# Performance work log

Hardware: AMD Instinct MI355X
Metric: run time of the kernel (lower is better)

The kernel has to match this reference:

```python
import jax, jax.numpy as jnp
import numpy as np

D_MODEL = 1024
N_HEADS = 16
D_K = 64
B = 2
S = 2048


def setup_inputs() -> dict:
    key = jax.random.key(0)
    ks = jax.random.split(key, 6)
    scale = 1.0 / np.sqrt(D_MODEL)
    x = jax.random.normal(ks[0], (B, S, D_MODEL), dtype=jnp.float32)
    Wq = jax.random.normal(ks[1], (D_MODEL, D_MODEL), dtype=jnp.float32) * scale
    Wk = jax.random.normal(ks[2], (D_MODEL, D_MODEL), dtype=jnp.float32) * scale
    Wv = jax.random.normal(ks[3], (D_MODEL, D_MODEL), dtype=jnp.float32) * scale
    Wo = jax.random.normal(ks[4], (D_MODEL, D_MODEL), dtype=jnp.float32) * scale
    bq = jnp.zeros((D_MODEL,), jnp.float32)
    bk = jnp.zeros((D_MODEL,), jnp.float32)
    bv = jnp.zeros((D_MODEL,), jnp.float32)
    bo = jnp.zeros((D_MODEL,), jnp.float32)
    # causal mask, broadcast over batch and heads: [1, 1, S, S]
    mask = jnp.tril(jnp.ones((S, S), jnp.int32))[None, None, :, :]
    return {"x": x, "mask": mask, "Wq": Wq, "bq": bq, "Wk": Wk, "bk": bk,
            "Wv": Wv, "bv": bv, "Wo": Wo, "bo": bo}


def reference(x, mask, Wq, bq, Wk, bk, Wv, bv, Wo, bo):
    b, s, _ = x.shape
    # projections (torch Linear: y = x @ W^T + b); split heads -> [b, h, s, d_k]
    def split_heads(y):
        return y.reshape(b, s, N_HEADS, D_K).transpose(0, 2, 1, 3)
    Q = split_heads(x @ Wq.T + bq)
    K = split_heads(x @ Wk.T + bk)
    V = split_heads(x @ Wv.T + bv)
    scores = jnp.einsum('bhqd,bhkd->bhqk', Q, K) / jnp.sqrt(jnp.float32(D_K))
    scores = jnp.where(mask == 0, -jnp.inf, scores)
    attn = jax.nn.softmax(scores, axis=-1)  # dropout p=0 -> identity
    out = jnp.einsum('bhqk,bhkd->bhqd', attn, V)
    out = out.transpose(0, 2, 1, 3).reshape(b, s, D_MODEL)
    return out @ Wo.T + bo
```

## Files before the change

kernel.cpp:

```cpp
#include <hip/hip_runtime.h>
#include <math.h>
#include <type_traits>

#define D_MODEL 1024
#define N_HEADS 16
#define D_KK    64
#define B_SZ    2
#define SEQ     2048
#define M_TOTAL (B_SZ * SEQ)

#define QSCALE 0.18033688011112042f

typedef __attribute__((ext_vector_type(8))) short short8;
typedef __attribute__((ext_vector_type(4))) float f32x4;

static __device__ __forceinline__ ushort f2bf(float f) {
    union { float f; unsigned u; } c; c.f = f;
    unsigned u = c.u;
    unsigned r = (u + 0x7fffu + ((u >> 16) & 1u)) >> 16;
    return (ushort)r;
}

static __device__ __forceinline__ unsigned packbf(float a, float b) {
    unsigned ua = __float_as_uint(a) + 0x8000u;
    unsigned ub = __float_as_uint(b) + 0x8000u;
    return __builtin_amdgcn_perm(ub, ua, 0x07060302u);
}

static __device__ __forceinline__ void gload16(const void* g, void* l) {
    __builtin_amdgcn_global_load_lds(
        (const __attribute__((address_space(1))) void*)g,
        (__attribute__((address_space(3))) void*)l, 16, 0, 0);
}

__global__ __launch_bounds__(256)
void cvt_kernel(const float* __restrict__ x,  const float* __restrict__ wq,
                const float* __restrict__ wk, const float* __restrict__ wv,
                const float* __restrict__ wo,
                ushort* __restrict__ xb,  ushort* __restrict__ wqb,
                ushort* __restrict__ wkb, ushort* __restrict__ wvb,
                ushort* __restrict__ wob)
{
    const float* s; ushort* d; int n4;
    switch (blockIdx.y) {
        case 0:  s = x;  d = xb;  n4 = M_TOTAL * D_MODEL / 4; break;
        case 1:  s = wq; d = wqb; n4 = D_MODEL * D_MODEL / 4; break;
        case 2:  s = wk; d = wkb; n4 = D_MODEL * D_MODEL / 4; break;
        case 3:  s = wv; d = wvb; n4 = D_MODEL * D_MODEL / 4; break;
        default: s = wo; d = wob; n4 = D_MODEL * D_MODEL / 4; break;
    }
    const int stride = gridDim.x * blockDim.x;
    for (int i = blockIdx.x * blockDim.x + threadIdx.x; i < n4; i += stride) {
        float4 v = reinterpret_cast<const float4*>(s)[i];
        ushort4 u;
        u.x = f2bf(v.x); u.y = f2bf(v.y); u.z = f2bf(v.z); u.w = f2bf(v.w);
        reinterpret_cast<ushort4*>(d)[i] = u;
    }
}

template<int EPI>
__global__ __launch_bounds__(256)
void gemm_mfma(const ushort* __restrict__ A,
               const ushort* __restrict__ W0, const float* __restrict__ b0, void* __restrict__ C0,
               const ushort* __restrict__ W1, const float* __restrict__ b1, void* __restrict__ C1,
               const ushort* __restrict__ W2, const float* __restrict__ b2, void* __restrict__ C2)
{
    constexpr int K = D_MODEL;

    const ushort* W    = W0;
    const float*  bias = b0;
    void*         C    = C0;
    if (blockIdx.z == 1) { W = W1; bias = b1; C = C1; }
    else if (blockIdx.z == 2) { W = W2; bias = b2; C = C2; }

    __shared__ ushort As[128 * 32];
    __shared__ ushort Bs[128 * 32];

    const int tid  = threadIdx.x;
    const int w    = tid >> 6;
    const int lane = tid & 63;
    const int lr   = lane & 15;
    const int lc   = lane >> 4;
    const int wr   = w >> 1;
    const int wc   = w & 1;
    const int m0   = blockIdx.x * 128;
    const int n0   = blockIdx.y * 128;

    const int srow = lane >> 2;
    const int scol = (lane & 3) * 8;
    const int g0   = w * 2;

    const ushort* gA = A + (size_t)(m0 + g0 * 16 + srow) * K + scol;
    const ushort* gB = W + (size_t)(n0 + g0 * 16 + srow) * K + scol;
    ushort* lA = &As[g0 * 512];
    ushort* lB = &Bs[g0 * 512];

    f32x4 acc[4][4];
#pragma unroll
    for (int m = 0; m < 4; ++m)
#pragma unroll
        for (int n = 0; n < 4; ++n) acc[m][n] = (f32x4)0.0f;

    for (int k0 = 0; k0 < K; k0 += 32) {
        gload16(gA + k0,          lA);
        gload16(gA + k0 + 16 * K, lA + 512);
        gload16(gB + k0,          lB);
        gload16(gB + k0 + 16 * K, lB + 512);
        __syncthreads();

        short8 af[4], bfr[4];
#pragma unroll
        for (int m = 0; m < 4; ++m)
            af[m] = *reinterpret_cast<const short8*>(
                &As[(wr * 64 + m * 16 + lr) * 32 + lc * 8]);
#pragma unroll
        for (int n = 0; n < 4; ++n)
            bfr[n] = *reinterpret_cast<const short8*>(
                &Bs[(wc * 64 + n * 16 + lr) * 32 + lc * 8]);
#pragma unroll
        for (int m = 0; m < 4; ++m)
#pragma unroll
            for (int n = 0; n < 4; ++n)
                acc[m][n] = __builtin_amdgcn_mfma_f32_16x16x32_bf16(
                    af[m], bfr[n], acc[m][n], 0, 0, 0);
        __syncthreads();
    }

    float bv[4];
#pragma unroll
    for (int n = 0; n < 4; ++n) bv[n] = bias[n0 + wc * 64 + n * 16 + lr];
    const int row_base = m0 + wr * 64;

    if (EPI == 0) {
        float* Cf = (float*)C;
#pragma unroll
        for (int m = 0; m < 4; ++m)
#pragma unroll
        for (int r = 0; r < 4; ++r) {
            const int row = row_base + m * 16 + lc * 4 + r;
#pragma unroll
            for (int n = 0; n < 4; ++n)
                Cf[(size_t)row * D_MODEL + n0 + wc * 64 + n * 16 + lr] =
                    acc[m][n][r] + bv[n];
        }
    } else {
        ushort* Cu = (ushort*)C;
        const bool vt  = (blockIdx.z == 2);
        const float osc = (blockIdx.z == 0) ? QSCALE : 1.0f;
#pragma unroll
        for (int m = 0; m < 4; ++m) {
            const int row4 = row_base + m * 16 + lc * 4;
            const int bb = row4 >> 11;
            const int ss = row4 & 2047;
            const size_t bhbase = (size_t)bb * N_HEADS;
#pragma unroll
            for (int n = 0; n < 4; ++n) {
                const int col = n0 + wc * 64 + n * 16 + lr;
                const int h = col >> 6, d = col & 63;
                if (vt) {
                    ushort4 u;
                    u.x = f2bf(acc[m][n][0] + bv[n]);
                    u.y = f2bf(acc[m][n][1] + bv[n]);
                    u.z = f2bf(acc[m][n][2] + bv[n]);
                    u.w = f2bf(acc[m][n][3] + bv[n]);
                    *reinterpret_cast<ushort4*>(
                        &Cu[((bhbase + h) * D_KK + d) * SEQ + ss]) = u;
                } else {
#pragma unroll
                    for (int r = 0; r < 4; ++r)
                        Cu[((bhbase + h) * SEQ + ss + r) * D_KK + d] =
                            f2bf((acc[m][n][r] + bv[n]) * osc);
                }
            }
        }
    }
}

__global__ __launch_bounds__(256, 4)
void attn_mfma_kernel(const ushort* __restrict__ Qb, const ushort* __restrict__ Kb,
                      const ushort* __restrict__ Vt, ushort* __restrict__ Ob)
{
    __shared__ ushort Ks[2][4096];
    __shared__ ushort Vs[2][4096];
    __shared__ ushort P_lds[4][1024];

    const int tid  = threadIdx.x;
    const int w    = tid >> 6;
    const int lane = tid & 63;
    const int lr   = lane & 15;
    const int lc   = lane >> 4;

    const int id  = blockIdx.x;
    const int xcd = id & 7;
    const int j   = id >> 3;
    const int bh  = xcd * 4 + (j & 3);
    const int qb  = 31 - (j >> 2);
    const int b   = bh >> 4;
    const int h   = bh & 15;
    const int q0  = qb * 64;
    const int qr0 = q0 + w * 16;
    const int nt  = qb + 1;

    const ushort* Kbase = Kb + (size_t)bh * SEQ * D_KK;
    const ushort* Vbase = Vt + (size_t)bh * D_KK * SEQ;

    const int rsub = lane >> 3;
    const int csw  = ((lane & 7) ^ rsub) << 3;

    ushort* Pw     = &P_lds[w][0];
    const int sw_w = (lr & 7) << 4;

    const ushort* Qp = Qb + ((size_t)bh * SEQ + qr0 + lr) * D_KK + lc * 8;
    const short8 qa0 = *reinterpret_cast<const short8*>(Qp);
    const short8 qa1 = *reinterpret_cast<const short8*>(Qp + 32);

    f32x4 acc_o[4];
#pragma unroll
    for (int t = 0; t < 4; ++t) acc_o[t] = (f32x4)0.0f;
    float m_run = -1e30f;
    float l_run = 0.0f;

#pragma unroll
    for (int cc = 0; cc < 2; ++cc) {
        const int c = w + cc * 4;
        gload16(Kbase + (size_t)(c * 8 + rsub) * D_KK + csw, &Ks[0][c * 512]);
        gload16(Vbase + (size_t)(c * 8 + rsub) * SEQ + csw,  &Vs[0][c * 512]);
    }
    __syncthreads();

    auto tile_body = [&](int buf, auto maskc) {
        constexpr bool MASK = decltype(maskc)::value;
        const ushort* Ksb = &Ks[buf][0];
        const ushort* Vsb = &Vs[buf][0];

        f32x4 s[4];
#pragma unroll
        for (int t = 0; t < 4; ++t) {
            const int rbyte = (t * 16 + lr) * 128;
            const short8 kb0 = *reinterpret_cast<const short8*>(
                &Ksb[(rbyte + ((lc * 16) ^ sw_w)) >> 1]);
            const short8 kb1 = *reinterpret_cast<const short8*>(
                &Ksb[(rbyte + ((64 + lc * 16) ^ sw_w)) >> 1]);
            f32x4 a = (f32x4)0.0f;
            a = __builtin_amdgcn_mfma_f32_16x16x32_bf16(kb0, qa0, a, 0, 0, 0);
            a = __builtin_amdgcn_mfma_f32_16x16x32_bf16(kb1, qa1, a, 0, 0, 0);
            s[t] = a;
        }

        float tmax = -1e30f;
#pragma unroll
        for (int t = 0; t < 4; ++t)
#pragma unroll
            for (int r = 0; r < 4; ++r) {
                if (MASK) {
                    const int kl = t * 16 + lc * 4 + r;
                    if (kl > w * 16 + lr) s[t][r] = -1e30f;
                }
                tmax = fmaxf(tmax, s[t][r]);
            }
        tmax = fmaxf(tmax, __shfl_xor(tmax, 16));
        tmax = fmaxf(tmax, __shfl_xor(tmax, 32));

        if (!__all(tmax <= m_run + 8.0f)) {
            const float mnew = fmaxf(m_run, tmax);
            const float corr = __builtin_amdgcn_exp2f(m_run - mnew);
            m_run = mnew;
            l_run *= corr;
            float cr[4];
#pragma unroll
            for (int r = 0; r < 4; ++r) cr[r] = __shfl(corr, lc * 4 + r, 16);
#pragma unroll
            for (int t = 0; t < 4; ++t)
#pragma unroll
                for (int r = 0; r < 4; ++r) acc_o[t][r] *= cr[r];
        }

        float rsum = 0.0f;
#pragma unroll
        for (int t = 0; t < 4; ++t) {
#pragma unroll
            for (int r = 0; r < 4; ++r) {
                const float p = __builtin_amdgcn_exp2f(s[t][r] - m_run);
                s[t][r] = p;
                rsum += p;
            }
            const unsigned lo = packbf(s[t][0], s[t][1]);
            const unsigned hi = packbf(s[t][2], s[t][3]);
            *reinterpret_cast<uint2*>(
                &Pw[(lr * 128 + ((t * 32 + lc * 8) ^ sw_w)) >> 1]) =
                make_uint2(lo, hi);
        }
        rsum += __shfl_xor(rsum, 16);
        rsum += __shfl_xor(rsum, 32);
        l_run += rsum;

        const short8 pa0 = *reinterpret_cast<const short8*>(
            &Pw[(lr * 128 + ((lc * 16) ^ sw_w)) >> 1]);
        const short8 pa1 = *reinterpret_cast<const short8*>(
            &Pw[(lr * 128 + ((64 + lc * 16) ^ sw_w)) >> 1]);

#pragma unroll
        for (int t = 0; t < 4; ++t) {
            const int rbyte = (t * 16 + lr) * 128;
            const short8 vb0 = *reinterpret_cast<const short8*>(
                &Vsb[(rbyte + ((lc * 16) ^ sw_w)) >> 1]);
            const short8 vb1 = *reinterpret_cast<const short8*>(
                &Vsb[(rbyte + ((64 + lc * 16) ^ sw_w)) >> 1]);
            acc_o[t] = __builtin_amdgcn_mfma_f32_16x16x32_bf16(
                    pa0, vb0, acc_o[t], 0, 0, 0);
            acc_o[t] = __builtin_amdgcn_mfma_f32_16x16x32_bf16(
                    pa1, vb1, acc_o[t], 0, 0, 0);
        }
    };

    int buf = 0;
    for (int it = 0; it < nt - 1; ++it) {
        const int kn = (it + 1) * 64;
#pragma unroll
        for (int cc = 0; cc < 2; ++cc) {
            const int c = w + cc * 4;
            gload16(Kbase + (size_t)(kn + c * 8 + rsub) * D_KK + csw,
                    &Ks[buf ^ 1][c * 512]);
            gload16(Vbase + (size_t)(c * 8 + rsub) * SEQ + kn + csw,
                    &Vs[buf ^ 1][c * 512]);
        }
        tile_body(buf, std::integral_constant<bool, false>{});
        __syncthreads();
        buf ^= 1;
    }
    tile_body(buf, std::integral_constant<bool, true>{});

    const float linv = 1.0f / l_run;
    float invr[4];
#pragma unroll
    for (int r = 0; r < 4; ++r) invr[r] = __shfl(linv, lc * 4 + r, 16);
#pragma unroll
    for (int r = 0; r < 4; ++r) {
        const int qrow = qr0 + lc * 4 + r;
        ushort* Op = Ob + ((size_t)b * SEQ + qrow) * D_MODEL + h * D_KK;
#pragma unroll
        for (int t = 0; t < 4; ++t)
            Op[t * 16 + lr] = f2bf(acc_o[t][r] * invr[r]);
    }
}

extern "C" void kernel_launch(void* const* d_in, const int* in_sizes, int n_in,
                              void* d_out, int out_size, void* d_ws, size_t ws_size,
                              hipStream_t stream)
{
    const float* x  = (const float*)d_in[0];
    const float* Wq = (const float*)d_in[2];
    const float* bq = (const float*)d_in[3];
    const float* Wk = (const float*)d_in[4];
    const float* bk = (const float*)d_in[5];
    const float* Wv = (const float*)d_in[6];
    const float* bv = (const float*)d_in[7];
    const float* Wo = (const float*)d_in[8];
    const float* bo = (const float*)d_in[9];
    float* out = (float*)d_out;

    const size_t TSZ = (size_t)M_TOTAL * D_MODEL;
    const size_t WSZ = (size_t)D_MODEL * D_MODEL;
    ushort* xb  = (ushort*)d_ws;
    ushort* Wqb = xb  + TSZ;
    ushort* Wkb = Wqb + WSZ;
    ushort* Wvb = Wkb + WSZ;
    ushort* Wob = Wvb + WSZ;
    ushort* Qb  = Wob + WSZ;
    ushort* Kb  = Qb  + TSZ;
    ushort* Vt  = Kb  + TSZ;
    ushort* Ob  = Vt  + TSZ;

    dim3 blk(256);
    cvt_kernel<<<dim3(256, 5), blk, 0, stream>>>(x, Wq, Wk, Wv, Wo,
                                                 xb, Wqb, Wkb, Wvb, Wob);

    dim3 g_qkv(M_TOTAL / 128, D_MODEL / 128, 3);
    gemm_mfma<1><<<g_qkv, blk, 0, stream>>>(xb, Wqb, bq, Qb,
                                                Wkb, bk, Kb,
                                                Wvb, bv, Vt);

    attn_mfma_kernel<<<dim3(1024), blk, 0, stream>>>(Qb, Kb, Vt, Ob);

    dim3 g_o(M_TOTAL / 128, D_MODEL / 128, 1);
    gemm_mfma<0><<<g_o, blk, 0, stream>>>(Ob, Wob, bo, out, Wob, bo, out, Wob, bo, out);
}
```

Measured before the change: 123.6 us.

## Double-buffer GEMM LDS tiles with swizzle, 128x64 tiles, and XCD-aware block mapping

Rewrites the projection GEMM main loop to use double-buffered LDS tiles with K=64 per stage. The next stage's global loads are issued before computing on the current buffer, and one barrier is dropped per iteration. The tile shape changes from 128x128 to 128x64, and an XOR swizzle is applied to the LDS layout to avoid bank conflicts. A 1D grid remaps blocks so each XCD works on a contiguous set of M tiles for L2 reuse. In exchange it uses more LDS per block, and the narrower tiles re-read A more often.

Result: faster. 106.3 us (-14.0%).

```diff
diff --git a/kernel.cpp b/kernel.cpp
--- a/kernel.cpp
+++ b/kernel.cpp
@@ -67,14 +67,25 @@
 {
     constexpr int K = D_MODEL;
 
+    __shared__ ushort As[2][128 * 64];
+    __shared__ ushort Bs[2][64 * 64];
+
+    const int id  = blockIdx.x;
+    const int xcd = id & 7;
+    const int j   = id >> 3;
+    const int mt  = xcd * 4 + (j & 3);
+    const int ntz = j >> 2;
+    const int nt  = ntz & 15;
+    const int z   = ntz >> 4;
+
     const ushort* W    = W0;
     const float*  bias = b0;
     void*         C    = C0;
-    if (blockIdx.z == 1) { W = W1; bias = b1; C = C1; }
-    else if (blockIdx.z == 2) { W = W2; bias = b2; C = C2; }
-
-    __shared__ ushort As[128 * 32];
-    __shared__ ushort Bs[128 * 32];
+    if (z == 1) { W = W1; bias = b1; C = C1; }
+    else if (z == 2) { W = W2; bias = b2; C = C2; }
+
+    const int m0 = mt * 128;
+    const int n0 = nt * 64;
 
     const int tid  = threadIdx.x;
     const int w    = tid >> 6;
@@ -83,52 +94,73 @@
     const int lc   = lane >> 4;
     const int wr   = w >> 1;
     const int wc   = w & 1;
-    const int m0   = blockIdx.x * 128;
-    const int n0   = blockIdx.y * 128;
-
-    const int srow = lane >> 2;
-    const int scol = (lane & 3) * 8;
-    const int g0   = w * 2;
-
-    const ushort* gA = A + (size_t)(m0 + g0 * 16 + srow) * K + scol;
-    const ushort* gB = W + (size_t)(n0 + g0 * 16 + srow) * K + scol;
-    ushort* lA = &As[g0 * 512];
-    ushort* lB = &Bs[g0 * 512];
-
-    f32x4 acc[4][4];
+
+    const int rsub = lane >> 3;
+    const int csw  = ((lane & 7) ^ rsub) << 3;
+
+    const ushort* gA = A + (size_t)(m0 + w * 8 + rsub) * K + csw;
+    const ushort* gB = W + (size_t)(n0 + w * 8 + rsub) * K + csw;
+
+    f32x4 acc[4][2];
 #pragma unroll
     for (int m = 0; m < 4; ++m)
 #pragma unroll
-        for (int n = 0; n < 4; ++n) acc[m][n] = (f32x4)0.0f;
-
-    for (int k0 = 0; k0 < K; k0 += 32) {
-        gload16(gA + k0,          lA);
-        gload16(gA + k0 + 16 * K, lA + 512);
-        gload16(gB + k0,          lB);
-        gload16(gB + k0 + 16 * K, lB + 512);
+        for (int n = 0; n < 2; ++n) acc[m][n] = (f32x4)0.0f;
+
+#pragma unroll
+    for (int ca = 0; ca < 4; ++ca)
+        gload16(gA + (size_t)(32 * ca) * K, &As[0][(w + 4 * ca) * 512]);
+#pragma unroll
+    for (int cb = 0; cb < 2; ++cb)
+        gload16(gB + (size_t)(32 * cb) * K, &Bs[0][(w + 4 * cb) * 512]);
+    __syncthreads();
+
+    const int swz = (lr & 7) << 4;
+    int buf = 0;
+    for (int it = 0; it < 16; ++it) {
+        if (it < 15) {
+            const int kn = (it + 1) * 64;
+#pragma unroll
+            for (int ca = 0; ca < 4; ++ca)
+                gload16(gA + (size_t)(32 * ca) * K + kn, &As[buf ^ 1][(w + 4 * ca) * 512]);
+#pragma unroll
+            for (int cb = 0; cb < 2; ++cb)
+                gload16(gB + (size_t)(32 * cb) * K + kn, &Bs[buf ^ 1][(w + 4 * cb) * 512]);
+        }
+
+        short8 af[4][2], bfr[2][2];
+#pragma unroll
+        for (int m = 0; m < 4; ++m) {
+            const int rbyte = (wr * 64 + m * 16 + lr) * 128;
+#pragma unroll
+            for (int kk = 0; kk < 2; ++kk)
+                af[m][kk] = *reinterpret_cast<const short8*>(
+                    &As[buf][(rbyte + ((kk * 64 + lc * 16) ^ swz)) >> 1]);
+        }
+#pragma unroll
+        for (int n = 0; n < 2; ++n) {
+            const int rbyte = (wc * 32 + n * 16 + lr) * 128;
+#pragma unroll
+            for (int kk = 0; kk < 2; ++kk)
+                bfr[n][kk] = *reinterpret_cast<const short8*>(
+                    &Bs[buf][(rbyte + ((kk * 64 + lc * 16) ^ swz)) >> 1]);
+        }
+#pragma unroll
+        for (int kk = 0; kk < 2; ++kk)
+#pragma unroll
+            for (int m = 0; m < 4; ++m)
+#pragma unroll
+                for (int n = 0; n < 2; ++n)
+                    acc[m][n] = __builtin_amdgcn_mfma_f32_16x16x32_bf16(
+                        af[m][kk], bfr[n][kk], acc[m][n], 0, 0, 0);
+
         __syncthreads();
-
-        short8 af[4], bfr[4];
-#pragma unroll
-        for (int m = 0; m < 4; ++m)
-            af[m] = *reinterpret_cast<const short8*>(
-                &As[(wr * 64 + m * 16 + lr) * 32 + lc * 8]);
-#pragma unroll
-        for (int n = 0; n < 4; ++n)
-            bfr[n] = *reinterpret_cast<const short8*>(
-                &Bs[(wc * 64 + n * 16 + lr) * 32 + lc * 8]);
-#pragma unroll
-        for (int m = 0; m < 4; ++m)
-#pragma unroll
-            for (int n = 0; n < 4; ++n)
-                acc[m][n] = __builtin_amdgcn_mfma_f32_16x16x32_bf16(
-                    af[m], bfr[n], acc[m][n], 0, 0, 0);
-        __syncthreads();
-    }
-
-    float bv[4];
-#pragma unroll
-    for (int n = 0; n < 4; ++n) bv[n] = bias[n0 + wc * 64 + n * 16 + lr];
+        buf ^= 1;
+    }
+
+    float bv[2];
+#pragma unroll
+    for (int n = 0; n < 2; ++n) bv[n] = bias[n0 + wc * 32 + n * 16 + lr];
     const int row_base = m0 + wr * 64;
 
     if (EPI == 0) {
@@ -139,14 +171,14 @@
         for (int r = 0; r < 4; ++r) {
             const int row = row_base + m * 16 + lc * 4 + r;
 #pragma unroll
-            for (int n = 0; n < 4; ++n)
-                Cf[(size_t)row * D_MODEL + n0 + wc * 64 + n * 16 + lr] =
+            for (int n = 0; n < 2; ++n)
+                Cf[(size_t)row * D_MODEL + n0 + wc * 32 + n * 16 + lr] =
                     acc[m][n][r] + bv[n];
         }
     } else {
         ushort* Cu = (ushort*)C;
-        const bool vt  = (blockIdx.z == 2);
-        const float osc = (blockIdx.z == 0) ? QSCALE : 1.0f;
+        const bool vt   = (z == 2);
+        const float osc = (z == 0) ? QSCALE : 1.0f;
 #pragma unroll
         for (int m = 0; m < 4; ++m) {
             const int row4 = row_base + m * 16 + lc * 4;
@@ -154,8 +186,8 @@
             const int ss = row4 & 2047;
             const size_t bhbase = (size_t)bb * N_HEADS;
 #pragma unroll
-            for (int n = 0; n < 4; ++n) {
-                const int col = n0 + wc * 64 + n * 16 + lr;
+            for (int n = 0; n < 2; ++n) {
+                const int col = n0 + wc * 32 + n * 16 + lr;
                 const int h = col >> 6, d = col & 63;
                 if (vt) {
                     ushort4 u;
@@ -375,13 +407,13 @@
     cvt_kernel<<<dim3(256, 5), blk, 0, stream>>>(x, Wq, Wk, Wv, Wo,
                                                  xb, Wqb, Wkb, Wvb, Wob);
 
-    dim3 g_qkv(M_TOTAL / 128, D_MODEL / 128, 3);
-    gemm_mfma<1><<<g_qkv, blk, 0, stream>>>(xb, Wqb, bq, Qb,
-                                                Wkb, bk, Kb,
-                                                Wvb, bv, Vt);
+    gemm_mfma<1><<<dim3(1536), blk, 0, stream>>>(xb, Wqb, bq, Qb,
+                                                     Wkb, bk, Kb,
+                                                     Wvb, bv, Vt);
 
     attn_mfma_kernel<<<dim3(1024), blk, 0, stream>>>(Qb, Kb, Vt, Ob);
 
-    dim3 g_o(M_TOTAL / 128, D_MODEL / 128, 1);
-    gemm_mfma<0><<<g_o, blk, 0, stream>>>(Ob, Wob, bo, out, Wob, bo, out, Wob, bo, out);
-}
+    gemm_mfma<0><<<dim3(512), blk, 0, stream>>>(Ob, Wob, bo, out,
+                                                    Wob, bo, out,
+                                                    Wob, bo, out);
+}
```
